# Performance work log

Measured on AMD Instinct MI355X. Metric: run time of the kernel, lower is better.

## Reference

```python
import jax, jax.numpy as jnp
import numpy as np

H = 128          # input hidden dim
HID = 128        # expert hidden width
OUT = 128        # out_channels
NR = 8           # n_routed
NS = 2           # n_shared
RDIM = 16        # router feature dim


def setup_inputs() -> dict:
    key = jax.random.key(0)
    ks = jax.random.split(key, 11)
    s = 0.05
    x = jax.random.normal(ks[0], (2, 32, 32, 32, H), dtype=jnp.float32)
    # router params
    Wr1 = jax.random.normal(ks[1], (H, RDIM), dtype=jnp.float32) * s
    br1 = jnp.zeros((RDIM,), dtype=jnp.float32)
    Wr2 = jax.random.normal(ks[2], (RDIM, NR), dtype=jnp.float32) * s
    br2 = jnp.zeros((NR,), dtype=jnp.float32)
    # routed expert params, stacked on leading expert axis
    We1 = jax.random.normal(ks[3], (NR, H, HID), dtype=jnp.float32) * s
    be1 = jnp.zeros((NR, HID), dtype=jnp.float32)
    We2 = jax.random.normal(ks[4], (NR, HID, OUT), dtype=jnp.float32) * s
    be2 = jnp.zeros((NR, OUT), dtype=jnp.float32)
    # shared expert params
    Ws1 = jax.random.normal(ks[5], (NS, H, HID), dtype=jnp.float32) * s
    bs1 = jnp.zeros((NS, HID), dtype=jnp.float32)
    Ws2 = jax.random.normal(ks[6], (NS, HID, OUT), dtype=jnp.float32) * s
    bs2 = jnp.zeros((NS, OUT), dtype=jnp.float32)
    return dict(x=x, Wr1=Wr1, br1=br1, Wr2=Wr2, br2=br2,
                We1=We1, be1=be1, We2=We2, be2=be2,
                Ws1=Ws1, bs1=bs1, Ws2=Ws2, bs2=bs2)


def reference(x, Wr1, br1, Wr2, br2, We1, be1, We2, be2, Ws1, bs1, Ws2, bs2):
    # router: Dense(16) -> relu -> Dense(n_routed) -> softmax
    rf = jax.nn.relu(jnp.einsum('...h,hr->...r', x, Wr1) + br1)
    logits = jnp.einsum('...r,re->...e', rf, Wr2) + br2
    gate = jax.nn.softmax(logits, axis=-1)                      # [..., NR]
    threshold = 1.0 / NR
    mask = (gate > threshold).astype(gate.dtype)
    mg = gate * mask
    mg = mg / (jnp.sum(mg, axis=-1, keepdims=True) + 1e-8)
    # routed experts (batched over expert axis e): Dense -> gelu(tanh) -> Dense
    hr = jax.nn.gelu(jnp.einsum('...h,ehd->...ed', x, We1) + be1)   # [..., NR, HID]
    ro = jnp.einsum('...ed,edo->...eo', hr, We2) + be2              # [..., NR, OUT]
    routed_agg = jnp.einsum('...eo,...e->...o', ro, mg)
    # shared experts summed
    hs = jax.nn.gelu(jnp.einsum('...h,ehd->...ed', x, Ws1) + bs1)   # [..., NS, HID]
    so = jnp.einsum('...ed,edo->...eo', hs, Ws2) + bs2              # [..., NS, OUT]
    shared_agg = jnp.sum(so, axis=-2)
    return routed_agg + shared_agg
```

## Files before the change

### kernel.cpp

```cpp
#include <hip/hip_runtime.h>
#include <hip/hip_bf16.h>

typedef __bf16 bf16x8 __attribute__((ext_vector_type(8)));
typedef float  f32x16 __attribute__((ext_vector_type(16)));
typedef float  f32x4  __attribute__((ext_vector_type(4)));
typedef float  f32x2  __attribute__((ext_vector_type(2)));

static __device__ __forceinline__ f32x16 mfma32(bf16x8 a, bf16x8 b, f32x16 c) {
    return __builtin_amdgcn_mfma_f32_32x32x16_bf16(a, b, c, 0, 0, 0);
}

#define GELU_C1 2.30220820f
#define GELU_C2 0.10294324f

__global__ __launch_bounds__(256) void pack_kernel(
    const float* __restrict__ We1, const float* __restrict__ be1,
    const float* __restrict__ Ws1, const float* __restrict__ bs1,
    const float* __restrict__ We2, const float* __restrict__ Ws2,
    __bf16* __restrict__ w1p, __bf16* __restrict__ w2p)
{
    int tid = blockIdx.x * 256 + threadIdx.x;
    if (tid < 23040) {
        int l  = tid & 63;
        int ks = (tid >> 6) % 9;
        int nt = (tid / 576) & 3;
        int e  = tid / 2304;
        const float* src = (e < 8) ? (We1 + e * 16384) : (Ws1 + (e - 8) * 16384);
        const float* bia = (e < 8) ? (be1 + e * 128)   : (bs1 + (e - 8) * 128);
        int n = nt * 32 + (l & 31);
        int kb = ks * 16 + (l >> 5) * 8;
        bf16x8 v;
        #pragma unroll
        for (int j = 0; j < 8; ++j) {
            int k = kb + j;
            float f = (k < 128) ? src[k * 128 + n] : ((k == 128) ? bia[n] : 0.f);
            v[j] = (__bf16)f;
        }
        *(bf16x8*)(w1p + (size_t)tid * 8) = v;
    } else if (tid < 43520) {
        int t2 = tid - 23040;
        int l  = t2 & 63;
        int ks = (t2 >> 6) & 7;
        int ot = (t2 / 512) & 3;
        int e  = t2 / 2048;
        const float* src = (e < 8) ? (We2 + e * 16384) : (Ws2 + (e - 8) * 16384);
        int o  = ot * 32 + (l & 31);
        int lh = l >> 5;
        bf16x8 v;
        #pragma unroll
        for (int j = 0; j < 8; ++j) {
            int hid = 16 * ks + 8 * (j >> 2) + 4 * lh + (j & 3);
            v[j] = (__bf16)src[hid * 128 + o];
        }
        *(bf16x8*)(w2p + (size_t)t2 * 8) = v;
    }
}

__global__ __launch_bounds__(256, 2) void moe_main_kernel(
    const float* __restrict__ x,
    const float* __restrict__ Wr1, const float* __restrict__ br1,
    const float* __restrict__ Wr2, const float* __restrict__ br2,
    const __bf16* __restrict__ w1p, const __bf16* __restrict__ w2p,
    const float* __restrict__ be2, const float* __restrict__ bs2,
    float* __restrict__ out)
{
    __shared__ __align__(16) char lds[62464];
    float*  xs  = (float*)lds;
    __bf16* Xp  = (__bf16*)(lds + 33792);
    double* rfs = (double*)(lds + 33792 + 18432);
    float*  mgs = (float*)(lds + 33792 + 18432 + 8192);
    float*  Red = (float*)lds;

    const int t    = threadIdx.x;
    const int lane = t & 63;
    const int wave = t >> 6;
    const int l31  = lane & 31;
    const int lh   = lane >> 5;
    const int mt   = wave >> 1;
    const int h    = wave & 1;
    const int tok0 = blockIdx.x * 64;

    #pragma unroll
    for (int i = 0; i < 4; ++i) {
        int g = i * 256 + t;
        int m = g >> 4;
        int c = g & 15;
        const f32x4* sp = (const f32x4*)(x + (size_t)(tok0 + m) * 128 + c * 8);
        f32x4 va = sp[0], vb = sp[1];
        *(f32x4*)&xs[m * 132 + c * 8]     = va;
        *(f32x4*)&xs[m * 132 + c * 8 + 4] = vb;
        bf16x8 v;
        v[0]=(__bf16)va[0]; v[1]=(__bf16)va[1]; v[2]=(__bf16)va[2]; v[3]=(__bf16)va[3];
        v[4]=(__bf16)vb[0]; v[5]=(__bf16)vb[1]; v[6]=(__bf16)vb[2]; v[7]=(__bf16)vb[3];
        *(bf16x8*)&Xp[(((m >> 5) * 9 + (c >> 1)) * 64 + (c & 1) * 32 + (m & 31)) * 8] = v;
    }
    if (t < 128) {
        int mtx = t >> 6, l = t & 63;
        bf16x8 v;
        #pragma unroll
        for (int j = 0; j < 8; ++j) v[j] = (__bf16)0.f;
        if (l < 32) v[0] = (__bf16)1.0f;
        *(bf16x8*)&Xp[((mtx * 9 + 8) * 64 + l) * 8] = v;
    }
    __syncthreads();

    {
        const int tok = t & 63;
        const int rq  = (t >> 6) * 4;
        double rf4[4];
        #pragma unroll
        for (int j = 0; j < 4; ++j) rf4[j] = (double)br1[rq + j];
        const f32x4* xr = (const f32x4*)(xs + tok * 132);
        for (int c = 0; c < 32; ++c) {
            f32x4 xv4 = xr[c];
            #pragma unroll
            for (int q = 0; q < 4; ++q) {
                double xv = (double)xv4[q];
                int k = c * 4 + q;
                #pragma unroll
                for (int j = 0; j < 4; ++j)
                    rf4[j] = fma(xv, (double)Wr1[k * 16 + rq + j], rf4[j]);
            }
        }
        #pragma unroll
        for (int j = 0; j < 4; ++j)
            rfs[tok * 16 + rq + j] = rf4[j] > 0.0 ? rf4[j] : 0.0;
    }
    __syncthreads();

    if (t < 64) {
        double lg[8];
        #pragma unroll
        for (int j = 0; j < 8; ++j) lg[j] = (double)br2[j];
        #pragma unroll
        for (int r = 0; r < 16; ++r) {
            double rv = rfs[t * 16 + r];
            #pragma unroll
            for (int j = 0; j < 8; ++j)
                lg[j] = fma(rv, (double)Wr2[r * 8 + j], lg[j]);
        }
        double mx = lg[0];
        #pragma unroll
        for (int j = 1; j < 8; ++j) mx = lg[j] > mx ? lg[j] : mx;
        double ex[8]; double s = 0.0;
        #pragma unroll
        for (int j = 0; j < 8; ++j) { ex[j] = exp(lg[j] - mx); s += ex[j]; }
        double mv[8]; double ms = 0.0;
        #pragma unroll
        for (int j = 0; j < 8; ++j) {
            double g = ex[j] / s;
            double m = (g > 0.125) ? g : 0.0;
            mv[j] = m; ms += m;
        }
        double inv = 1.0 / (ms + 1e-8);
        #pragma unroll
        for (int j = 0; j < 8; ++j) mgs[t * 8 + j] = (float)(mv[j] * inv);
    }
    __syncthreads();

    const float* mgr = mgs + (32 * mt + l31) * 8;
    f32x4 ga4 = *(const f32x4*)mgr;
    f32x4 gb4 = *(const f32x4*)(mgr + 4);
    float gte[8] = {ga4[0], ga4[1], ga4[2], ga4[3], gb4[0], gb4[1], gb4[2], gb4[3]};

    f32x16 acc[4];
    #pragma unroll
    for (int ot = 0; ot < 4; ++ot)
        #pragma unroll
        for (int i = 0; i < 16; ++i) acc[ot][i] = 0.f;

    const bf16x8* w1v = (const bf16x8*)w1p;
    const bf16x8* w2v = (const bf16x8*)w2p;

    #pragma unroll 1
    for (int e = 0; e < 10; ++e) {
        const bf16x8* wap = w1v + ((size_t)(e * 4 + 2 * h) * 9) * 64 + lane;
        bf16x8 wa[9], wb[9];
        #pragma unroll
        for (int ks = 0; ks < 9; ++ks) { wa[ks] = wap[ks * 64]; wb[ks] = wap[(9 + ks) * 64]; }

        const bf16x8* wBp = w2v + ((size_t)(e * 4) * 8 + 4 * h) * 64 + lane;
        bf16x8 wB[4][4];
        #pragma unroll
        for (int ot = 0; ot < 4; ++ot)
            #pragma unroll
            for (int kq = 0; kq < 4; ++kq)
                wB[ot][kq] = wBp[(ot * 8 + kq) * 64];

        f32x16 a1[2];
        #pragma unroll
        for (int n2 = 0; n2 < 2; ++n2)
            #pragma unroll
            for (int i = 0; i < 16; ++i) a1[n2][i] = 0.f;

        #pragma unroll
        for (int ks = 0; ks < 9; ++ks) {
            bf16x8 xb = *(const bf16x8*)&Xp[((mt * 9 + ks) * 64 + lane) * 8];
            a1[0] = mfma32(wa[ks], xb, a1[0]);
            a1[1] = mfma32(wb[ks], xb, a1[1]);
        }

        const float gv = (e < 8) ? gte[e] : 1.0f;

        #pragma unroll
        for (int n2 = 0; n2 < 2; ++n2) {
            #pragma unroll
            for (int b = 0; b < 2; ++b) {
                bf16x8 fr;
                #pragma unroll
                for (int jp = 0; jp < 4; ++jp) {
                    f32x2 hh; hh[0] = a1[n2][8 * b + 2 * jp]; hh[1] = a1[n2][8 * b + 2 * jp + 1];
                    f32x2 tt = hh * hh;
                    f32x2 pp;
                    pp[0] = fmaf(tt[0], -GELU_C2, -GELU_C1);
                    pp[1] = fmaf(tt[1], -GELU_C2, -GELU_C1);
                    f32x2 mm = hh * pp;
                    float e0 = __builtin_amdgcn_exp2f(mm[0]);
                    float e1 = __builtin_amdgcn_exp2f(mm[1]);
                    float q0 = __builtin_amdgcn_rcpf(1.f + e0);
                    float q1 = __builtin_amdgcn_rcpf(1.f + e1);
                    f32x2 gg; gg[0] = hh[0] * q0 * gv; gg[1] = hh[1] * q1 * gv;
                    fr[2 * jp]     = (__bf16)gg[0];
                    fr[2 * jp + 1] = (__bf16)gg[1];
                }
                int kq = 2 * n2 + b;
                acc[0] = mfma32(fr, wB[0][kq], acc[0]);
                acc[1] = mfma32(fr, wB[1][kq], acc[1]);
                acc[2] = mfma32(fr, wB[2][kq], acc[2]);
                acc[3] = mfma32(fr, wB[3][kq], acc[3]);
            }
        }
    }

    __syncthreads();
    if (h == 1) {
        #pragma unroll
        for (int ot = 0; ot < 4; ++ot)
            #pragma unroll
            for (int r = 0; r < 16; ++r)
                Red[((mt * 4 + ot) * 16 + r) * 64 + lane] = acc[ot][r];
    }
    __syncthreads();
    if (h == 0) {
        float be2c[4][8], bsc[4];
        #pragma unroll
        for (int ot = 0; ot < 4; ++ot) {
            int o = 32 * ot + l31;
            bsc[ot] = bs2[o] + bs2[128 + o];
            #pragma unroll
            for (int ee = 0; ee < 8; ++ee) be2c[ot][ee] = be2[ee * 128 + o];
        }
        const float* mgb = mgs + (32 * mt) * 8;
        #pragma unroll
        for (int r = 0; r < 16; ++r) {
            int mrow = (r & 3) + 8 * (r >> 2) + 4 * lh;
            f32x4 g0 = *(const f32x4*)&mgb[mrow * 8];
            f32x4 g1 = *(const f32x4*)&mgb[mrow * 8 + 4];
            size_t orow = (size_t)(tok0 + 32 * mt + mrow) * 128;
            #pragma unroll
            for (int ot = 0; ot < 4; ++ot) {
                float b = bsc[ot];
                #pragma unroll
                for (int ee = 0; ee < 4; ++ee) b = fmaf(g0[ee], be2c[ot][ee], b);
                #pragma unroll
                for (int ee = 0; ee < 4; ++ee) b = fmaf(g1[ee], be2c[ot][4 + ee], b);
                float v = acc[ot][r] + Red[((mt * 4 + ot) * 16 + r) * 64 + lane] + b;
                out[orow + 32 * ot + l31] = v;
            }
        }
    }
}

extern "C" void kernel_launch(void* const* d_in, const int* in_sizes, int n_in,
                              void* d_out, int out_size, void* d_ws, size_t ws_size,
                              hipStream_t stream)
{
    const float* x   = (const float*)d_in[0];
    const float* Wr1 = (const float*)d_in[1];
    const float* br1 = (const float*)d_in[2];
    const float* Wr2 = (const float*)d_in[3];
    const float* br2 = (const float*)d_in[4];
    const float* We1 = (const float*)d_in[5];
    const float* be1 = (const float*)d_in[6];
    const float* We2 = (const float*)d_in[7];
    const float* be2 = (const float*)d_in[8];
    const float* Ws1 = (const float*)d_in[9];
    const float* bs1 = (const float*)d_in[10];
    const float* Ws2 = (const float*)d_in[11];
    const float* bs2 = (const float*)d_in[12];

    __bf16* w1p = (__bf16*)d_ws;
    __bf16* w2p = (__bf16*)((char*)d_ws + 368640);

    pack_kernel<<<170, 256, 0, stream>>>(We1, be1, Ws1, bs1, We2, Ws2, w1p, w2p);
    moe_main_kernel<<<1024, 256, 0, stream>>>(x, Wr1, br1, Wr2, br2,
                                              w1p, w2p, be2, bs2, (float*)d_out);
}
```

Measured before the change: 200.1 us.

## Prefetch expert weights across iterations and precompute router weights in double

The expert loop is restructured to process one 32-column hidden tile at a time. It double-buffers the first-layer weight fragments in registers, prefetching the next tile while the current GELU and second-layer MFMAs run, and loads only the second-layer fragments needed per half. Router weights and biases are converted to double once in the pack kernel, so the main kernel skips per-element float-to-double conversion. Router reads use a wave-uniform index, the x stage uses a 130-float row stride with 8-byte accesses, and the softmax masking drops the per-element divide. Register pressure and numerical equivalence of the rescaled normalisation are the risks.

```diff
diff --git a/kernel.cpp b/kernel.cpp
--- a/kernel.cpp
+++ b/kernel.cpp
@@ -17,7 +17,11 @@
     const float* __restrict__ We1, const float* __restrict__ be1,
     const float* __restrict__ Ws1, const float* __restrict__ bs1,
     const float* __restrict__ We2, const float* __restrict__ Ws2,
-    __bf16* __restrict__ w1p, __bf16* __restrict__ w2p)
+    const float* __restrict__ Wr1, const float* __restrict__ br1,
+    const float* __restrict__ Wr2, const float* __restrict__ br2,
+    __bf16* __restrict__ w1p, __bf16* __restrict__ w2p,
+    double* __restrict__ wr1d, double* __restrict__ br1d,
+    double* __restrict__ wr2d, double* __restrict__ br2d)
 {
     int tid = blockIdx.x * 256 + threadIdx.x;
     if (tid < 23040) {
@@ -53,22 +57,34 @@
             v[j] = (__bf16)src[hid * 128 + o];
         }
         *(bf16x8*)(w2p + (size_t)t2 * 8) = v;
+    } else if (tid < 45568) {
+        int i = tid - 43520;
+        wr1d[i] = (double)Wr1[i];
+    } else if (tid < 45696) {
+        int i = tid - 45568;
+        wr2d[i] = (double)Wr2[i];
+    } else if (tid < 45712) {
+        int i = tid - 45696;
+        br1d[i] = (double)br1[i];
+    } else if (tid < 45720) {
+        int i = tid - 45712;
+        br2d[i] = (double)br2[i];
     }
 }
 
 __global__ __launch_bounds__(256, 2) void moe_main_kernel(
     const float* __restrict__ x,
-    const float* __restrict__ Wr1, const float* __restrict__ br1,
-    const float* __restrict__ Wr2, const float* __restrict__ br2,
+    const double* __restrict__ wr1d, const double* __restrict__ br1d,
+    const double* __restrict__ wr2d, const double* __restrict__ br2d,
     const __bf16* __restrict__ w1p, const __bf16* __restrict__ w2p,
     const float* __restrict__ be2, const float* __restrict__ bs2,
     float* __restrict__ out)
 {
-    __shared__ __align__(16) char lds[62464];
+    __shared__ __align__(16) char lds[61952];
     float*  xs  = (float*)lds;
-    __bf16* Xp  = (__bf16*)(lds + 33792);
-    double* rfs = (double*)(lds + 33792 + 18432);
-    float*  mgs = (float*)(lds + 33792 + 18432 + 8192);
+    __bf16* Xp  = (__bf16*)(lds + 33280);
+    double* rfs = (double*)(lds + 51712);
+    float*  mgs = (float*)(lds + 59904);
     float*  Red = (float*)lds;
 
     const int t    = threadIdx.x;
@@ -87,8 +103,12 @@
         int c = g & 15;
         const f32x4* sp = (const f32x4*)(x + (size_t)(tok0 + m) * 128 + c * 8);
         f32x4 va = sp[0], vb = sp[1];
-        *(f32x4*)&xs[m * 132 + c * 8]     = va;
-        *(f32x4*)&xs[m * 132 + c * 8 + 4] = vb;
+        float* xd = xs + m * 130 + c * 8;
+        f32x2 s0, s1, s2, s3;
+        s0[0]=va[0]; s0[1]=va[1]; s1[0]=va[2]; s1[1]=va[3];
+        s2[0]=vb[0]; s2[1]=vb[1]; s3[0]=vb[2]; s3[1]=vb[3];
+        *(f32x2*)(xd)     = s0; *(f32x2*)(xd + 2) = s1;
+        *(f32x2*)(xd + 4) = s2; *(f32x2*)(xd + 6) = s3;
         bf16x8 v;
         v[0]=(__bf16)va[0]; v[1]=(__bf16)va[1]; v[2]=(__bf16)va[2]; v[3]=(__bf16)va[3];
         v[4]=(__bf16)vb[0]; v[5]=(__bf16)vb[1]; v[6]=(__bf16)vb[2]; v[7]=(__bf16)vb[3];
@@ -107,19 +127,21 @@
     {
         const int tok = t & 63;
         const int rq  = (t >> 6) * 4;
+        const int rqs = __builtin_amdgcn_readfirstlane(rq);
         double rf4[4];
         #pragma unroll
-        for (int j = 0; j < 4; ++j) rf4[j] = (double)br1[rq + j];
-        const f32x4* xr = (const f32x4*)(xs + tok * 132);
-        for (int c = 0; c < 32; ++c) {
-            f32x4 xv4 = xr[c];
-            #pragma unroll
-            for (int q = 0; q < 4; ++q) {
-                double xv = (double)xv4[q];
-                int k = c * 4 + q;
+        for (int j = 0; j < 4; ++j) rf4[j] = br1d[rqs + j];
+        const float* xr = xs + tok * 130;
+        #pragma unroll 4
+        for (int c = 0; c < 64; ++c) {
+            f32x2 xv2 = *(const f32x2*)(xr + c * 2);
+            #pragma unroll
+            for (int q = 0; q < 2; ++q) {
+                double xv = (double)xv2[q];
+                int k = c * 2 + q;
                 #pragma unroll
                 for (int j = 0; j < 4; ++j)
-                    rf4[j] = fma(xv, (double)Wr1[k * 16 + rq + j], rf4[j]);
+                    rf4[j] = fma(xv, wr1d[k * 16 + rqs + j], rf4[j]);
             }
         }
         #pragma unroll
@@ -131,13 +153,13 @@
     if (t < 64) {
         double lg[8];
         #pragma unroll
-        for (int j = 0; j < 8; ++j) lg[j] = (double)br2[j];
+        for (int j = 0; j < 8; ++j) lg[j] = br2d[j];
         #pragma unroll
         for (int r = 0; r < 16; ++r) {
             double rv = rfs[t * 16 + r];
             #pragma unroll
             for (int j = 0; j < 8; ++j)
-                lg[j] = fma(rv, (double)Wr2[r * 8 + j], lg[j]);
+                lg[j] = fma(rv, wr2d[r * 8 + j], lg[j]);
         }
         double mx = lg[0];
         #pragma unroll
@@ -145,16 +167,17 @@
         double ex[8]; double s = 0.0;
         #pragma unroll
         for (int j = 0; j < 8; ++j) { ex[j] = exp(lg[j] - mx); s += ex[j]; }
-        double mv[8]; double ms = 0.0;
+        double ms = 0.0;
+        bool mk[8];
         #pragma unroll
         for (int j = 0; j < 8; ++j) {
-            double g = ex[j] / s;
-            double m = (g > 0.125) ? g : 0.0;
-            mv[j] = m; ms += m;
-        }
-        double inv = 1.0 / (ms + 1e-8);
-        #pragma unroll
-        for (int j = 0; j < 8; ++j) mgs[t * 8 + j] = (float)(mv[j] * inv);
+            mk[j] = (8.0 * ex[j] > s);
+            ms += mk[j] ? ex[j] : 0.0;
+        }
+        double inv = 1.0 / (ms + s * 1e-8);
+        #pragma unroll
+        for (int j = 0; j < 8; ++j)
+            mgs[t * 8 + j] = mk[j] ? (float)(ex[j] * inv) : 0.f;
     }
     __syncthreads();
 
@@ -172,44 +195,49 @@
     const bf16x8* w1v = (const bf16x8*)w1p;
     const bf16x8* w2v = (const bf16x8*)w2p;
 
+    bf16x8 wbuf[2][9];
+    {
+        const bf16x8* p = w1v + ((size_t)(2 * h) * 9) * 64 + lane;
+        #pragma unroll
+        for (int ks = 0; ks < 9; ++ks) wbuf[0][ks] = p[ks * 64];
+    }
+
     #pragma unroll 1
     for (int e = 0; e < 10; ++e) {
-        const bf16x8* wap = w1v + ((size_t)(e * 4 + 2 * h) * 9) * 64 + lane;
-        bf16x8 wa[9], wb[9];
-        #pragma unroll
-        for (int ks = 0; ks < 9; ++ks) { wa[ks] = wap[ks * 64]; wb[ks] = wap[(9 + ks) * 64]; }
-
-        const bf16x8* wBp = w2v + ((size_t)(e * 4) * 8 + 4 * h) * 64 + lane;
-        bf16x8 wB[4][4];
-        #pragma unroll
-        for (int ot = 0; ot < 4; ++ot)
-            #pragma unroll
-            for (int kq = 0; kq < 4; ++kq)
-                wB[ot][kq] = wBp[(ot * 8 + kq) * 64];
-
-        f32x16 a1[2];
-        #pragma unroll
-        for (int n2 = 0; n2 < 2; ++n2)
-            #pragma unroll
-            for (int i = 0; i < 16; ++i) a1[n2][i] = 0.f;
-
-        #pragma unroll
-        for (int ks = 0; ks < 9; ++ks) {
-            bf16x8 xb = *(const bf16x8*)&Xp[((mt * 9 + ks) * 64 + lane) * 8];
-            a1[0] = mfma32(wa[ks], xb, a1[0]);
-            a1[1] = mfma32(wb[ks], xb, a1[1]);
-        }
-
         const float gv = (e < 8) ? gte[e] : 1.0f;
-
         #pragma unroll
         for (int n2 = 0; n2 < 2; ++n2) {
+            const bf16x8* wBp = w2v + ((size_t)(e * 4) * 8 + 4 * h + 2 * n2) * 64 + lane;
+            bf16x8 wBc[8];
+            #pragma unroll
+            for (int ot = 0; ot < 4; ++ot)
+                #pragma unroll
+                for (int b = 0; b < 2; ++b)
+                    wBc[ot * 2 + b] = wBp[(ot * 8 + b) * 64];
+
+            f32x16 a1;
+            #pragma unroll
+            for (int i = 0; i < 16; ++i) a1[i] = 0.f;
+            #pragma unroll
+            for (int ks = 0; ks < 9; ++ks) {
+                bf16x8 xb = *(const bf16x8*)&Xp[((mt * 9 + ks) * 64 + lane) * 8];
+                a1 = mfma32(wbuf[n2][ks], xb, a1);
+            }
+
+            {
+                int en  = (n2 == 0) ? e : (e < 9 ? e + 1 : 9);
+                int ntn = (n2 == 0) ? (2 * h + 1) : (2 * h);
+                const bf16x8* p = w1v + ((size_t)(en * 4 + ntn) * 9) * 64 + lane;
+                #pragma unroll
+                for (int ks = 0; ks < 9; ++ks) wbuf[n2 ^ 1][ks] = p[ks * 64];
+            }
+
             #pragma unroll
             for (int b = 0; b < 2; ++b) {
                 bf16x8 fr;
                 #pragma unroll
                 for (int jp = 0; jp < 4; ++jp) {
-                    f32x2 hh; hh[0] = a1[n2][8 * b + 2 * jp]; hh[1] = a1[n2][8 * b + 2 * jp + 1];
+                    f32x2 hh; hh[0] = a1[8 * b + 2 * jp]; hh[1] = a1[8 * b + 2 * jp + 1];
                     f32x2 tt = hh * hh;
                     f32x2 pp;
                     pp[0] = fmaf(tt[0], -GELU_C2, -GELU_C1);
@@ -223,11 +251,10 @@
                     fr[2 * jp]     = (__bf16)gg[0];
                     fr[2 * jp + 1] = (__bf16)gg[1];
                 }
-                int kq = 2 * n2 + b;
-                acc[0] = mfma32(fr, wB[0][kq], acc[0]);
-                acc[1] = mfma32(fr, wB[1][kq], acc[1]);
-                acc[2] = mfma32(fr, wB[2][kq], acc[2]);
-                acc[3] = mfma32(fr, wB[3][kq], acc[3]);
+                acc[0] = mfma32(fr, wBc[0 * 2 + b], acc[0]);
+                acc[1] = mfma32(fr, wBc[1 * 2 + b], acc[1]);
+                acc[2] = mfma32(fr, wBc[2 * 2 + b], acc[2]);
+                acc[3] = mfma32(fr, wBc[3 * 2 + b], acc[3]);
             }
         }
     }
@@ -289,10 +316,16 @@
     const float* Ws2 = (const float*)d_in[11];
     const float* bs2 = (const float*)d_in[12];
 
-    __bf16* w1p = (__bf16*)d_ws;
-    __bf16* w2p = (__bf16*)((char*)d_ws + 368640);
-
-    pack_kernel<<<170, 256, 0, stream>>>(We1, be1, Ws1, bs1, We2, Ws2, w1p, w2p);
-    moe_main_kernel<<<1024, 256, 0, stream>>>(x, Wr1, br1, Wr2, br2,
+    __bf16* w1p  = (__bf16*)d_ws;
+    __bf16* w2p  = (__bf16*)((char*)d_ws + 368640);
+    double* wr1d = (double*)((char*)d_ws + 696320);
+    double* wr2d = (double*)((char*)d_ws + 712704);
+    double* br1d = (double*)((char*)d_ws + 713728);
+    double* br2d = (double*)((char*)d_ws + 713856);
+
+    pack_kernel<<<179, 256, 0, stream>>>(We1, be1, Ws1, bs1, We2, Ws2,
+                                         Wr1, br1, Wr2, br2,
+                                         w1p, w2p, wr1d, br1d, wr2d, br2d);
+    moe_main_kernel<<<1024, 256, 0, stream>>>(x, wr1d, br1d, wr2d, br2d,
                                               w1p, w2p, be2, bs2, (float*)d_out);
 }
```

New measurement: 176.5 us. -11.8%, faster.
